# Performance work log

Hardware: AMD Instinct MI355X
Metric: run time of the kernel (lower is better)

## Reference

```python
import jax, jax.numpy as jnp
import numpy as np

N_HEADS = 16
LOCAL_WINDOW = 512
ROPE_BASE = 10000.0


def _rotate_half(x):
    # interleaved rotate: out[..., 2i] = -x[..., 2i+1], out[..., 2i+1] = x[..., 2i]
    x1 = x[..., 0::2]
    x2 = x[..., 1::2]
    return jnp.stack((-x2, x1), axis=-1).reshape(x.shape)


def _rope_cache(T, hd, dtype):
    half = hd // 2
    inv_freq = 1.0 / (ROPE_BASE ** (jnp.arange(half, dtype=dtype) / half))
    t = jnp.arange(T, dtype=dtype)
    freqs = t[:, None] * inv_freq[None, :]  # [T, half]
    cos = jnp.repeat(jnp.cos(freqs), 2, axis=-1)  # [T, hd]
    sin = jnp.repeat(jnp.sin(freqs), 2, axis=-1)
    return cos, sin


def setup_inputs() -> dict:
    key = jax.random.key(0)
    k1, k2, k3, k4 = jax.random.split(key, 4)
    B, T, C = 2, 2048, 1024
    x = jax.random.normal(k1, (B, T, C), dtype=jnp.float32)
    Wqkv = jax.random.normal(k2, (3 * C, C), dtype=jnp.float32) * 0.02
    Wproj = jax.random.normal(k3, (C, C), dtype=jnp.float32) * 0.02
    bproj = jax.random.normal(k4, (C,), dtype=jnp.float32) * 0.02
    return {"x": x, "Wqkv": Wqkv, "Wproj": Wproj, "bproj": bproj}


def reference(x, Wqkv, Wproj, bproj):
    B, T, C = x.shape
    H = N_HEADS
    hd = C // H
    qkv = (x @ Wqkv.T).reshape(B, T, 3, H, hd).transpose(2, 0, 3, 1, 4)  # [3,B,H,T,hd]
    q, k, v = qkv[0], qkv[1], qkv[2]
    cos, sin = _rope_cache(T, hd, x.dtype)
    cos = cos[None, None]  # [1,1,T,hd]
    sin = sin[None, None]
    q = q * cos + _rotate_half(q) * sin
    k = k * cos + _rotate_half(k) * sin
    scale = 1.0 / jnp.sqrt(jnp.asarray(hd, dtype=x.dtype))
    scores = jnp.einsum('bhqd,bhkd->bhqk', q, k) * scale  # [B,H,T,T]
    i = jnp.arange(T)[:, None]
    j = jnp.arange(T)[None, :]
    allow = (j <= i) & (jnp.abs(i - j) <= LOCAL_WINDOW)  # causal & local band
    scores = jnp.where(allow[None, None], scores, jnp.asarray(-jnp.inf, dtype=x.dtype))
    attn = jax.nn.softmax(scores, axis=-1)
    y = jnp.einsum('bhqk,bhkd->bhqd', attn, v)  # [B,H,T,hd]
    y = y.transpose(0, 2, 1, 3).reshape(B, T, C)
    return y @ Wproj.T + bproj
```

## Files before the change

kernel.cpp:

```cpp
#include <hip/hip_runtime.h>
#include <math.h>

#define B_   2
#define T_   2048
#define C_   1024
#define H_   16
#define HD_  64
#define WIN_ 512
#define BT_  (B_ * T_)

typedef __bf16 bf16x8 __attribute__((ext_vector_type(8)));
typedef float  f32x4  __attribute__((ext_vector_type(4)));
typedef unsigned int u32x2 __attribute__((ext_vector_type(2)));
typedef unsigned short u16x8 __attribute__((ext_vector_type(8)));

__device__ __forceinline__ f32x4 mfma16(bf16x8 a, bf16x8 b, f32x4 c) {
    return __builtin_amdgcn_mfma_f32_16x16x32_bf16(a, b, c, 0, 0, 0);
}
__device__ __forceinline__ unsigned short f2b(float f) {
    __bf16 h = (__bf16)f;
    unsigned short u;
    __builtin_memcpy(&u, &h, 2);
    return u;
}
__device__ __forceinline__ void async_copy16(__bf16* lds, const __bf16* g) {
    __builtin_amdgcn_global_load_lds(
        (const __attribute__((address_space(1))) void*)g,
        (__attribute__((address_space(3))) void*)lds,
        16, 0, 0);
}

#define TR16(dst, va, OFFLIT) \
    asm volatile("ds_read_b64_tr_b16 %0, %1 offset:" OFFLIT : "=v"(dst) : "v"(va))

__device__ __forceinline__ bf16x8 combine_tr(u32x2 a, u32x2 b) {
    union { unsigned u[4]; bf16x8 v; } x;
    x.u[0] = a[0]; x.u[1] = a[1]; x.u[2] = b[0]; x.u[3] = b[1];
    return x.v;
}

#define VMW(n) asm volatile("s_waitcnt vmcnt(" #n ")" ::: "memory")

__global__ void prep_k(const float* __restrict__ x, const float* __restrict__ Wqkv,
                       const float* __restrict__ Wproj,
                       __bf16* __restrict__ xb, __bf16* __restrict__ Wqkvb,
                       __bf16* __restrict__ Wprojb,
                       float* __restrict__ cosT, float* __restrict__ sinT) {
    const int gid = blockIdx.x * 256 + threadIdx.x;
    const int N0 = BT_ * 1024 / 8;
    const int N1 = N0 + 3072 * 1024 / 8;
    const int N2 = N1 + 1024 * 1024 / 8;
    const int N3 = N2 + T_ * 32 / 8;
    if (gid < N2) {
        const float* src; __bf16* dst; int off;
        if (gid < N0)      { src = x;     dst = xb;     off = gid; }
        else if (gid < N1) { src = Wqkv;  dst = Wqkvb;  off = gid - N0; }
        else               { src = Wproj; dst = Wprojb; off = gid - N1; }
        float4 a = *(const float4*)&src[(size_t)off * 8];
        float4 b = *(const float4*)&src[(size_t)off * 8 + 4];
        bf16x8 o;
        o[0] = (__bf16)a.x; o[1] = (__bf16)a.y; o[2] = (__bf16)a.z; o[3] = (__bf16)a.w;
        o[4] = (__bf16)b.x; o[5] = (__bf16)b.y; o[6] = (__bf16)b.z; o[7] = (__bf16)b.w;
        *(bf16x8*)&dst[(size_t)off * 8] = o;
    } else if (gid < N3) {
        const int r = gid - N2;
        #pragma unroll
        for (int e = 0; e < 8; ++e) {
            int idx = r * 8 + e;
            int t = idx >> 5, j = idx & 31;
            float inv = powf(10000.0f, -(float)j / 32.0f);
            float f = (float)t * inv;
            cosT[idx] = cosf(f);
            sinT[idx] = sinf(f);
        }
    }
}

template<bool OUT_BF16, bool ROPE>
__global__ __launch_bounds__(256) void gemm_bt_mfma(
        const __bf16* __restrict__ A, const __bf16* __restrict__ Bm,
        const float* __restrict__ bias, void* __restrict__ Cv,
        int M, int N, int K,
        const float* __restrict__ cosT, const float* __restrict__ sinT)
{
    __shared__ __bf16 sA[3][128 * 32];
    __shared__ __bf16 sB[3][128 * 32];
    const int tid  = threadIdx.x;
    const int w    = tid >> 6;
    const int lane = tid & 63;
    const int c    = lane & 15;
    const int g    = lane >> 4;
    const int bm0  = blockIdx.y * 128;
    const int bn0  = blockIdx.x * 128;
    const int wm0  = (w >> 1) * 64;
    const int wn0  = (w & 1) * 64;

    f32x4 acc[4][4] = {};

    auto stage = [&](int buf, int k0) {
        #pragma unroll
        for (int it = 0; it < 2; ++it) {
            int s   = it * 256 + tid;
            int row = s >> 2;
            int col = ((s & 3) ^ ((row >> 1) & 3)) * 8;
            async_copy16(&sA[buf][s * 8], &A[(size_t)(bm0 + row) * K + k0 + col]);
            async_copy16(&sB[buf][s * 8], &Bm[(size_t)(bn0 + row) * K + k0 + col]);
        }
    };

    const int NT = K >> 5;
    stage(0, 0);
    stage(1, 32);

    for (int t = 0; t < NT; ++t) {
        if (t + 1 < NT) { VMW(4); } else { VMW(0); }
        __builtin_amdgcn_sched_barrier(0);
        __builtin_amdgcn_s_barrier();
        if (t + 2 < NT) {
            int fill = t + 2; while (fill >= 3) fill -= 3;
            stage(fill, (t + 2) * 32);
        }
        int cons = t; while (cons >= 3) cons -= 3;
        const __bf16* cA = sA[cons];
        const __bf16* cB = sB[cons];
        bf16x8 af[4], bfr[4];
        #pragma unroll
        for (int m = 0; m < 4; ++m) {
            int r = wm0 + m * 16 + c;
            af[m] = *(const bf16x8*)&cA[r * 32 + ((g ^ ((r >> 1) & 3)) * 8)];
        }
        #pragma unroll
        for (int n = 0; n < 4; ++n) {
            int r = wn0 + n * 16 + c;
            bfr[n] = *(const bf16x8*)&cB[r * 32 + ((g ^ ((r >> 1) & 3)) * 8)];
        }
        __builtin_amdgcn_s_setprio(1);
        #pragma unroll
        for (int m = 0; m < 4; ++m)
            #pragma unroll
            for (int n = 0; n < 4; ++n)
                acc[m][n] = mfma16(af[m], bfr[n], acc[m][n]);
        __builtin_amdgcn_s_setprio(0);
    }

    if (ROPE) {
        #pragma unroll
        for (int m = 0; m < 4; ++m) {
            #pragma unroll
            for (int r2 = 0; r2 < 4; ++r2) {
                const int row = bm0 + wm0 + m * 16 + g * 4 + r2;
                const int t = row & (T_ - 1);
                #pragma unroll
                for (int n = 0; n < 4; ++n) {
                    const int cbase = bn0 + wn0 + n * 16;
                    const int cc = cbase + c;
                    float v = acc[m][n][r2];
                    float outv;
                    if (cbase < 2048) {
                        float prt = __shfl_xor(v, 1);
                        int jj = (cc & 63) >> 1;
                        float cs = cosT[t * 32 + jj];
                        float sn = sinT[t * 32 + jj];
                        outv = (cc & 1) ? (v * cs + prt * sn) : (v * cs - prt * sn);
                    } else {
                        outv = v;
                    }
                    ((__bf16*)Cv)[(size_t)row * N + cc] = (__bf16)outv;
                }
            }
        }
    } else {
        #pragma unroll
        for (int m = 0; m < 4; ++m) {
            int rr = bm0 + wm0 + m * 16 + g * 4;
            #pragma unroll
            for (int n = 0; n < 4; ++n) {
                int cc = bn0 + wn0 + n * 16 + c;
                float bv = (!OUT_BF16 && bias) ? bias[cc] : 0.f;
                #pragma unroll
                for (int r2 = 0; r2 < 4; ++r2) {
                    float v = acc[m][n][r2] + bv;
                    if (OUT_BF16) ((__bf16*)Cv)[(size_t)(rr + r2) * N + cc] = (__bf16)v;
                    else          ((float*)Cv)[(size_t)(rr + r2) * N + cc] = v;
                }
            }
        }
    }
}

__global__ __launch_bounds__(256) void attn_k(const __bf16* __restrict__ qkv,
                                              __bf16* __restrict__ y)
{
    __shared__ __align__(16) unsigned short Ks[64 * 72];
    __shared__ __align__(16) unsigned short Ps[64 * 72];
    __shared__ __align__(16) unsigned short Vs[4 * 1040];

    const int tid  = threadIdx.x;
    const int lane = tid & 63;
    const int w    = tid >> 6;
    const int c    = lane & 15;
    const int g    = lane >> 4;

    const int bid = blockIdx.x;
    const int swz = (bid & 7) * 128 + (bid >> 3);
    const int q0 = (swz & 31) * 64;
    const int hb = swz >> 5;
    const int h  = hb & 15;
    const int b  = hb >> 4;

    bf16x8 qa[2];
    {
        const int qrow = q0 + w * 16 + c;
        const __bf16* qp = qkv + (size_t)(b * T_ + qrow) * 3072 + h * 64 + g * 8;
        bf16x8 r0 = *(const bf16x8*)qp;
        bf16x8 r1 = *(const bf16x8*)(qp + 32);
        #pragma unroll
        for (int e = 0; e < 8; ++e) {
            qa[0][e] = (__bf16)((float)r0[e] * 0.125f);
            qa[1][e] = (__bf16)((float)r1[e] * 0.125f);
        }
    }

    float m_run[4] = {-1e30f, -1e30f, -1e30f, -1e30f};
    float l_run[4] = {0.f, 0.f, 0.f, 0.f};
    f32x4 o[4] = {};

    unsigned vs_lane;
    {
        auto* p3 = (__attribute__((address_space(3))) const unsigned short*)Vs;
        vs_lane = (unsigned)(unsigned long long)p3 + (unsigned)(g * 256 + c * 8);
    }

    const int r0s = tid >> 3,          d80 = (tid & 7) * 8;
    const int r1s = (tid + 256) >> 3,  d81 = d80;
    const size_t kbase = (size_t)(b * T_) * 3072 + 1024 + h * 64;

    const int j_start = (q0 >= WIN_) ? (q0 - WIN_) : 0;

    u16x8 kr0, kr1, vr0, vr1;
    {
        const __bf16* p0 = qkv + kbase + (size_t)(j_start + r0s) * 3072 + d80;
        const __bf16* p1 = qkv + kbase + (size_t)(j_start + r1s) * 3072 + d81;
        kr0 = *(const u16x8*)p0;  vr0 = *(const u16x8*)(p0 + 1024);
        kr1 = *(const u16x8*)p1;  vr1 = *(const u16x8*)(p1 + 1024);
    }

    for (int j0 = j_start; j0 <= q0; j0 += 64) {
        __syncthreads();
        {
            union { u16x8 v; ushort4 h[2]; } u;
            u.v = kr0;
            *(ushort4*)&Ks[r0s * 72 + d80]     = u.h[0];
            *(ushort4*)&Ks[r0s * 72 + d80 + 4] = u.h[1];
            u.v = kr1;
            *(ushort4*)&Ks[r1s * 72 + d81]     = u.h[0];
            *(ushort4*)&Ks[r1s * 72 + d81 + 4] = u.h[1];
            *(u16x8*)&Vs[(d80 >> 4) * 1040 + r0s * 16 + (d80 & 15)] = vr0;
            *(u16x8*)&Vs[(d81 >> 4) * 1040 + r1s * 16 + (d81 & 15)] = vr1;
        }
        __syncthreads();

        if (j0 + 64 <= q0) {
            const __bf16* p0 = qkv + kbase + (size_t)(j0 + 64 + r0s) * 3072 + d80;
            const __bf16* p1 = qkv + kbase + (size_t)(j0 + 64 + r1s) * 3072 + d81;
            kr0 = *(const u16x8*)p0;  vr0 = *(const u16x8*)(p0 + 1024);
            kr1 = *(const u16x8*)p1;  vr1 = *(const u16x8*)(p1 + 1024);
        }

        f32x4 sc[4];
        __builtin_amdgcn_s_setprio(1);
        #pragma unroll
        for (int nt = 0; nt < 4; ++nt) {
            const bf16x8 b0 = *(const bf16x8*)&Ks[(nt * 16 + c) * 72 + g * 8];
            const bf16x8 b1 = *(const bf16x8*)&Ks[(nt * 16 + c) * 72 + 32 + g * 8];
            f32x4 s = {0.f, 0.f, 0.f, 0.f};
            s = mfma16(qa[0], b0, s);
            s = mfma16(qa[1], b1, s);
            sc[nt] = s;
        }
        __builtin_amdgcn_s_setprio(0);

        const int rlo = q0 + w * 16;
        const bool need_mask = (j0 + 63 > rlo) || (rlo + 15 - j0 > WIN_);
        if (need_mask) {
            #pragma unroll
            for (int reg = 0; reg < 4; ++reg) {
                const int i_abs = rlo + g * 4 + reg;
                #pragma unroll
                for (int nt = 0; nt < 4; ++nt) {
                    int j_abs = j0 + nt * 16 + c;
                    bool ok = (j_abs <= i_abs) && (i_abs - j_abs <= WIN_);
                    sc[nt][reg] = ok ? sc[nt][reg] : -1e30f;
                }
            }
        }

        float pmax[4];
        #pragma unroll
        for (int reg = 0; reg < 4; ++reg) {
            float bm = fmaxf(fmaxf(sc[0][reg], sc[1][reg]), fmaxf(sc[2][reg], sc[3][reg]));
            #pragma unroll
            for (int off = 1; off < 16; off <<= 1)
                bm = fmaxf(bm, __shfl_xor(bm, off));
            pmax[reg] = bm;
        }
        int need = 0;
        #pragma unroll
        for (int reg = 0; reg < 4; ++reg)
            need |= (pmax[reg] > m_run[reg] + 8.f) ? 1 : 0;
        if (__any(need)) {
            #pragma unroll
            for (int reg = 0; reg < 4; ++reg) {
                float mn = fmaxf(m_run[reg], pmax[reg]);
                float corr = __expf(m_run[reg] - mn);
                m_run[reg] = mn;
                l_run[reg] *= corr;
                #pragma unroll
                for (int dt = 0; dt < 4; ++dt) o[dt][reg] *= corr;
            }
        }
        #pragma unroll
        for (int reg = 0; reg < 4; ++reg) {
            #pragma unroll
            for (int nt = 0; nt < 4; ++nt) {
                float p = __expf(sc[nt][reg] - m_run[reg]);
                l_run[reg] += p;
                Ps[(w * 16 + g * 4 + reg) * 72 + nt * 16 + c] = f2b(p);
            }
        }

        const bf16x8 pa0 = *(const bf16x8*)&Ps[(w * 16 + c) * 72 + g * 8];
        const bf16x8 pa1 = *(const bf16x8*)&Ps[(w * 16 + c) * 72 + 32 + g * 8];
        u32x2 t0[4], t1[4], t2[4], t3[4];
        #pragma unroll
        for (int dt = 0; dt < 4; ++dt) {
            unsigned va = vs_lane + dt * 2080;
            TR16(t0[dt], va, "0");
            TR16(t1[dt], va, "128");
            TR16(t2[dt], va, "1024");
            TR16(t3[dt], va, "1152");
        }
        asm volatile("s_waitcnt lgkmcnt(0)" ::: "memory");
        __builtin_amdgcn_sched_barrier(0);
        __builtin_amdgcn_s_setprio(1);
        #pragma unroll
        for (int dt = 0; dt < 4; ++dt) {
            bf16x8 vb0 = combine_tr(t0[dt], t1[dt]);
            bf16x8 vb1 = combine_tr(t2[dt], t3[dt]);
            o[dt] = mfma16(pa0, vb0, o[dt]);
            o[dt] = mfma16(pa1, vb1, o[dt]);
        }
        __builtin_amdgcn_s_setprio(0);
    }

    float inv_l[4];
    #pragma unroll
    for (int reg = 0; reg < 4; ++reg) {
        float L = l_run[reg];
        #pragma unroll
        for (int off = 1; off < 16; off <<= 1)
            L += __shfl_xor(L, off);
        inv_l[reg] = 1.f / L;
    }
    #pragma unroll
    for (int dt = 0; dt < 4; ++dt)
        #pragma unroll
        for (int reg = 0; reg < 4; ++reg) {
            size_t row = (size_t)(b * T_ + q0 + w * 16 + g * 4 + reg);
            y[row * 1024 + h * 64 + dt * 16 + c] = (__bf16)(o[dt][reg] * inv_l[reg]);
        }
}

extern "C" void kernel_launch(void* const* d_in, const int* in_sizes, int n_in,
                              void* d_out, int out_size, void* d_ws, size_t ws_size,
                              hipStream_t stream) {
    const float* x     = (const float*)d_in[0];
    const float* Wqkv  = (const float*)d_in[1];
    const float* Wproj = (const float*)d_in[2];
    const float* bproj = (const float*)d_in[3];
    float* out = (float*)d_out;

    char* p = (char*)d_ws;
    float*  cosT   = (float*)p;   p += (size_t)T_ * 32 * 4;
    float*  sinT   = (float*)p;   p += (size_t)T_ * 32 * 4;
    __bf16* xb     = (__bf16*)p;  p += (size_t)BT_ * 1024 * 2;
    __bf16* Wqkvb  = (__bf16*)p;  p += (size_t)3072 * 1024 * 2;
    __bf16* Wprojb = (__bf16*)p;  p += (size_t)1024 * 1024 * 2;
    __bf16* qkvb   = (__bf16*)p;  p += (size_t)BT_ * 3072 * 2;
    __bf16* yb     = (__bf16*)p;  p += (size_t)BT_ * 1024 * 2;

    const int nprep = (BT_ * 1024 + 3072 * 1024 + 1024 * 1024) / 8 + T_ * 32 / 8;
    prep_k<<<(nprep + 255) / 256, 256, 0, stream>>>(
        x, Wqkv, Wproj, xb, Wqkvb, Wprojb, cosT, sinT);

    dim3 g1(3072 / 128, BT_ / 128);
    gemm_bt_mfma<true, true><<<g1, 256, 0, stream>>>(
        xb, Wqkvb, nullptr, qkvb, BT_, 3072, 1024, cosT, sinT);

    attn_k<<<(T_ / 64) * H_ * B_, 256, 0, stream>>>(qkvb, yb);

    dim3 g2(1024 / 128, BT_ / 128);
    gemm_bt_mfma<false, false><<<g2, 256, 0, stream>>>(
        yb, Wprojb, bproj, out, BT_, 1024, 1024, nullptr, nullptr);
}
```

Baseline: 125.6 us.

## Use 256x256-tile 512-thread GEMM with block swizzle for QKV projection

Adds a dedicated QKV projection kernel that computes 256x256 output tiles with 8 waves, each holding 128x64 accumulators, instead of 128x128 tiles with 4 waves. It also remaps block IDs in an XCD-style swizzle so that neighbouring tiles are grouped. Larger tiles raise arithmetic intensity and cut global and L2 traffic per FLOP. The costs are higher register pressure (32 accumulators per wave), 96KB of LDS, and only 192 blocks, which may leave some of the CUs underused. The old templated GEMM is reduced to the fp32-output projection path.

```diff
diff --git a/kernel.cpp b/kernel.cpp
--- a/kernel.cpp
+++ b/kernel.cpp
@@ -76,12 +76,109 @@
     }
 }
 
-template<bool OUT_BF16, bool ROPE>
+__global__ __launch_bounds__(512, 2) void gemm256_qkv(
+        const __bf16* __restrict__ A, const __bf16* __restrict__ Bm,
+        __bf16* __restrict__ C, int M, int N, int K,
+        const float* __restrict__ cosT, const float* __restrict__ sinT)
+{
+    __shared__ __bf16 sA[3][256 * 32];
+    __shared__ __bf16 sB[3][256 * 32];
+
+    const int tid  = threadIdx.x;
+    const int w    = tid >> 6;
+    const int lane = tid & 63;
+    const int c    = lane & 15;
+    const int g    = lane >> 4;
+
+    const int nbx = N >> 8;
+    const int cpx = gridDim.x >> 3;
+    const int bid = blockIdx.x;
+    const int swz = (bid & 7) * cpx + (bid >> 3);
+    const int bm0 = (swz / nbx) << 8;
+    const int bn0 = (swz % nbx) << 8;
+    const int wm0 = (w >> 2) << 7;
+    const int wn0 = (w & 3) << 6;
+
+    f32x4 acc[8][4] = {};
+
+    auto stage = [&](int buf, int k0) {
+        #pragma unroll
+        for (int it = 0; it < 2; ++it) {
+            int s   = it * 512 + tid;
+            int row = s >> 2;
+            int col = ((s & 3) ^ ((row >> 1) & 3)) * 8;
+            async_copy16(&sA[buf][s * 8], &A[(size_t)(bm0 + row) * K + k0 + col]);
+            async_copy16(&sB[buf][s * 8], &Bm[(size_t)(bn0 + row) * K + k0 + col]);
+        }
+    };
+
+    const int NT = K >> 5;
+    stage(0, 0);
+    stage(1, 32);
+
+    int cons = 0;
+    for (int t = 0; t < NT; ++t) {
+        if (t + 1 < NT) { VMW(4); } else { VMW(0); }
+        __builtin_amdgcn_sched_barrier(0);
+        __builtin_amdgcn_s_barrier();
+        if (t + 2 < NT) {
+            int fill = cons + 2; if (fill >= 3) fill -= 3;
+            stage(fill, (t + 2) << 5);
+        }
+        const __bf16* cA = sA[cons];
+        const __bf16* cB = sB[cons];
+        bf16x8 af[8], bfr[4];
+        #pragma unroll
+        for (int m = 0; m < 8; ++m) {
+            int r = wm0 + m * 16 + c;
+            af[m] = *(const bf16x8*)&cA[r * 32 + ((g ^ ((r >> 1) & 3)) * 8)];
+        }
+        #pragma unroll
+        for (int n = 0; n < 4; ++n) {
+            int r = wn0 + n * 16 + c;
+            bfr[n] = *(const bf16x8*)&cB[r * 32 + ((g ^ ((r >> 1) & 3)) * 8)];
+        }
+        __builtin_amdgcn_s_setprio(1);
+        #pragma unroll
+        for (int m = 0; m < 8; ++m)
+            #pragma unroll
+            for (int n = 0; n < 4; ++n)
+                acc[m][n] = mfma16(af[m], bfr[n], acc[m][n]);
+        __builtin_amdgcn_s_setprio(0);
+        cons = (cons + 1 == 3) ? 0 : cons + 1;
+    }
+
+    #pragma unroll
+    for (int m = 0; m < 8; ++m) {
+        #pragma unroll
+        for (int r2 = 0; r2 < 4; ++r2) {
+            const int row = bm0 + wm0 + m * 16 + g * 4 + r2;
+            const int t = row & (T_ - 1);
+            #pragma unroll
+            for (int n = 0; n < 4; ++n) {
+                const int cbase = bn0 + wn0 + n * 16;
+                const int cc = cbase + c;
+                float v = acc[m][n][r2];
+                float outv;
+                if (cbase < 2048) {
+                    float prt = __shfl_xor(v, 1);
+                    int jj = (cc & 63) >> 1;
+                    float cs = cosT[t * 32 + jj];
+                    float sn = sinT[t * 32 + jj];
+                    outv = (cc & 1) ? (v * cs + prt * sn) : (v * cs - prt * sn);
+                } else {
+                    outv = v;
+                }
+                C[(size_t)row * N + cc] = (__bf16)outv;
+            }
+        }
+    }
+}
+
 __global__ __launch_bounds__(256) void gemm_bt_mfma(
         const __bf16* __restrict__ A, const __bf16* __restrict__ Bm,
-        const float* __restrict__ bias, void* __restrict__ Cv,
-        int M, int N, int K,
-        const float* __restrict__ cosT, const float* __restrict__ sinT)
+        const float* __restrict__ bias, float* __restrict__ Cv,
+        int M, int N, int K)
 {
     __shared__ __bf16 sA[3][128 * 32];
     __shared__ __bf16 sB[3][128 * 32];
@@ -143,47 +240,16 @@
         __builtin_amdgcn_s_setprio(0);
     }
 
-    if (ROPE) {
-        #pragma unroll
-        for (int m = 0; m < 4; ++m) {
-            #pragma unroll
-            for (int r2 = 0; r2 < 4; ++r2) {
-                const int row = bm0 + wm0 + m * 16 + g * 4 + r2;
-                const int t = row & (T_ - 1);
-                #pragma unroll
-                for (int n = 0; n < 4; ++n) {
-                    const int cbase = bn0 + wn0 + n * 16;
-                    const int cc = cbase + c;
-                    float v = acc[m][n][r2];
-                    float outv;
-                    if (cbase < 2048) {
-                        float prt = __shfl_xor(v, 1);
-                        int jj = (cc & 63) >> 1;
-                        float cs = cosT[t * 32 + jj];
-                        float sn = sinT[t * 32 + jj];
-                        outv = (cc & 1) ? (v * cs + prt * sn) : (v * cs - prt * sn);
-                    } else {
-                        outv = v;
-                    }
-                    ((__bf16*)Cv)[(size_t)row * N + cc] = (__bf16)outv;
-                }
-            }
-        }
-    } else {
-        #pragma unroll
-        for (int m = 0; m < 4; ++m) {
-            int rr = bm0 + wm0 + m * 16 + g * 4;
-            #pragma unroll
-            for (int n = 0; n < 4; ++n) {
-                int cc = bn0 + wn0 + n * 16 + c;
-                float bv = (!OUT_BF16 && bias) ? bias[cc] : 0.f;
-                #pragma unroll
-                for (int r2 = 0; r2 < 4; ++r2) {
-                    float v = acc[m][n][r2] + bv;
-                    if (OUT_BF16) ((__bf16*)Cv)[(size_t)(rr + r2) * N + cc] = (__bf16)v;
-                    else          ((float*)Cv)[(size_t)(rr + r2) * N + cc] = v;
-                }
-            }
+    #pragma unroll
+    for (int m = 0; m < 4; ++m) {
+        int rr = bm0 + wm0 + m * 16 + g * 4;
+        #pragma unroll
+        for (int n = 0; n < 4; ++n) {
+            int cc = bn0 + wn0 + n * 16 + c;
+            float bv = bias ? bias[cc] : 0.f;
+            #pragma unroll
+            for (int r2 = 0; r2 < 4; ++r2)
+                Cv[(size_t)(rr + r2) * N + cc] = acc[m][n][r2] + bv;
         }
     }
 }
@@ -393,13 +459,11 @@
     prep_k<<<(nprep + 255) / 256, 256, 0, stream>>>(
         x, Wqkv, Wproj, xb, Wqkvb, Wprojb, cosT, sinT);
 
-    dim3 g1(3072 / 128, BT_ / 128);
-    gemm_bt_mfma<true, true><<<g1, 256, 0, stream>>>(
-        xb, Wqkvb, nullptr, qkvb, BT_, 3072, 1024, cosT, sinT);
+    gemm256_qkv<<<(BT_ / 256) * (3072 / 256), 512, 0, stream>>>(
+        xb, Wqkvb, qkvb, BT_, 3072, 1024, cosT, sinT);
 
     attn_k<<<(T_ / 64) * H_ * B_, 256, 0, stream>>>(qkvb, yb);
 
     dim3 g2(1024 / 128, BT_ / 128);
-    gemm_bt_mfma<false, false><<<g2, 256, 0, stream>>>(
-        yb, Wprojb, bproj, out, BT_, 1024, 1024, nullptr, nullptr);
-}
+    gemm_bt_mfma<<<g2, 256, 0, stream>>>(yb, Wprojb, bproj, out, BT_, 1024, 1024);
+}
```

After: 143.7 us. +14.4%, slower.
